# Performance work log

Hardware: AMD Instinct MI355X
Metric: run time of the kernel (lower is better)

The kernel has to match this reference:

```python
import jax, jax.numpy as jnp
import numpy as np

B, N, C_IN, C_OUT, BASIS = 8, 128, 64, 64, 15
AVG_NOBJ = 49.0
NEG_SLOPE = 0.01  # torch LeakyReLU default


def eops_2_to_2_sum(x, average_nobj=AVG_NOBJ):
    """x: [B, C, N, N] -> [B, C, 15, N, N].
    5 order-zero ops + 10 sum-aggregation ops (sums normalized by average_nobj,
    double sums by average_nobj**2, as in PELICAN's 'sum' aggregation)."""
    n = x.shape[-1]
    eye = jnp.eye(n, dtype=x.dtype)                       # [N, N]
    d = jnp.diagonal(x, axis1=-2, axis2=-1)               # [B, C, N]
    rowsum = x.sum(-1) / average_nobj                      # [B, C, N]
    colsum = x.sum(-2) / average_nobj                      # [B, C, N]
    trace = d.sum(-1) / average_nobj                       # [B, C]
    allsum = x.sum((-2, -1)) / (average_nobj ** 2)         # [B, C]
    bc = lambda v: jnp.broadcast_to(v, x.shape)
    ops = [
        # --- order zero (no aggregation) ---
        d[..., :, None] * eye,                 # diag(A) embedded on diagonal
        bc(d[..., :, None]),                   # A_ii broadcast along j
        bc(d[..., None, :]),                   # A_jj broadcast along i
        x,                                     # identity
        jnp.swapaxes(x, -1, -2),               # transpose
        # --- aggregation ops ---
        rowsum[..., :, None] * eye,            # row sums on diagonal
        colsum[..., :, None] * eye,            # col sums on diagonal
        trace[..., None, None] * eye,          # trace on diagonal
        allsum[..., None, None] * eye,         # total sum on diagonal
        bc(rowsum[..., :, None]),              # rowsum_i broadcast along j
        bc(rowsum[..., None, :]),              # rowsum_j broadcast along i
        bc(colsum[..., :, None]),              # colsum_i broadcast along j
        bc(colsum[..., None, :]),              # colsum_j broadcast along i
        bc(trace[..., None, None]),            # trace broadcast everywhere
        bc(allsum[..., None, None]),           # total sum broadcast everywhere
    ]
    return jnp.stack(ops, axis=2)              # [B, C, 15, N, N]


def setup_inputs() -> dict:
    key = jax.random.key(0)
    ks = jax.random.split(key, 5)
    inputs = jax.random.normal(ks[0], (B, N, N, C_IN), jnp.float32)
    mask = jnp.ones((B, N, N, 1), jnp.float32)
    nobj = jnp.full((B,), float(N), jnp.float32)
    s_b = float(np.sqrt(1.0 / BASIS))
    s_d = float(np.sqrt(1.0 / C_IN))
    coefs00 = jax.random.normal(ks[1], (C_IN, BASIS), jnp.float32) * s_b
    coefs01 = jax.random.normal(ks[2], (C_OUT, BASIS), jnp.float32) * s_b
    coefs10 = jax.random.normal(ks[3], (C_IN, C_OUT), jnp.float32) * s_d
    coefs11 = jax.random.normal(ks[4], (C_IN, C_OUT), jnp.float32) * s_d
    bias = jnp.zeros((C_OUT,), jnp.float32)
    diag_bias = jnp.zeros((C_OUT,), jnp.float32)
    return {"inputs": inputs, "mask": mask, "nobj": nobj,
            "coefs00": coefs00, "coefs01": coefs01,
            "coefs10": coefs10, "coefs11": coefs11,
            "bias": bias, "diag_bias": diag_bias}


def reference(inputs, mask, nobj, coefs00, coefs01, coefs10, coefs11, bias, diag_bias):
    # inputs: [B, N, N, C_in] -> channels-first for basis construction
    x = jnp.transpose(inputs, (0, 3, 1, 2))                     # [B, C, N, N]
    ops = eops_2_to_2_sum(x)                                    # [B, C, 15, N, N]
    # low-rank reconstructed coefficient tensor [C_in, C_out, 15]
    coefs = (coefs00[:, None, :] * coefs10[:, :, None]
             + coefs01[None, :, :] * coefs11[:, :, None])
    out = jnp.einsum('dsb,ndbij->nijs', coefs, ops)             # [B, N, N, C_out]
    eye = jnp.eye(inputs.shape[1], dtype=out.dtype)[None, :, :, None]
    out = out + bias[None, None, None, :] + eye * diag_bias[None, None, None, :]
    out = jax.nn.leaky_relu(out, NEG_SLOPE)
    return out * mask
```

## Files before the change

### kernel.cpp

```cpp
#include <hip/hip_runtime.h>

#define BB 8
#define NN 128
#define CC 64
static constexpr float INV_A = 1.0f / 49.0f;

#define OFF_C    0
#define OFF_CB   61440
#define OFF_RS   65536
#define OFF_CS   131072
#define OFF_DV   196608
#define OFF_U1   263168
#define OFF_U2   328704
#define OFF_DG   394240
#define OFF_XT   459776
#define OFF_TR   4654080
#define OFF_AS   4654592

typedef __attribute__((ext_vector_type(8))) short v8s;
typedef __attribute__((ext_vector_type(4))) float v4f;

static __device__ inline unsigned pack2bf(float a, float b) {
    union { float f; unsigned u; } ua, ub; ua.f = a; ub.f = b;
    return ((ua.u + 0x8000u) >> 16) | ((ub.u + 0x8000u) & 0xffff0000u);
}
static __device__ inline unsigned short f2bf(float a) {
    union { float f; unsigned u; } ua; ua.f = a;
    return (unsigned short)((ua.u + 0x8000u) >> 16);
}

__global__ void k_pre(const float* __restrict__ in,
                      const float* __restrict__ c00, const float* __restrict__ c01,
                      const float* __restrict__ c10, const float* __restrict__ c11,
                      float* __restrict__ ws) {
    if (blockIdx.x >= 512) {
        int idx = (blockIdx.x - 512) * 256 + threadIdx.x;
        if (idx < 15 * 4096) {
            int b = idx >> 12; int r = idx & 4095; int d = r >> 6; int s = r & 63;
            ws[OFF_C + idx] = c00[d * 15 + b] * c10[d * 64 + s] + c01[s * 15 + b] * c11[d * 64 + s];
        } else if (idx < 15 * 4096 + 8192) {
            int k = idx - 15 * 4096;
            int which = k >> 12;
            int r = k & 4095; int s = r >> 6; int d = r & 63;
            int b = 3 + which;
            float v = c00[d * 15 + b] * c10[d * 64 + s] + c01[s * 15 + b] * c11[d * 64 + s];
            unsigned short* cb = (unsigned short*)(ws + OFF_CB);
            cb[s * 128 + which * 64 + d] = f2bf(v);
        }
        return;
    }
    __shared__ float4 part[4][4][16];
    int mode = blockIdx.x >> 8;
    int bb = blockIdx.x & 255;
    int n = bb >> 5; int g0 = (bb & 31) * 4;
    int t = threadIdx.x;
    int q = t >> 6; int ii = (t >> 4) & 3; int d4 = t & 15;
    float4 acc = make_float4(0.f, 0.f, 0.f, 0.f);
    if (mode == 0) {
        int i = g0 + ii;
        float4 dvv = acc; bool hd = false;
        const float* base = in + ((size_t)(n * NN + i)) * NN * CC + d4 * 4;
        for (int j = q * 32; j < q * 32 + 32; ++j) {
            float4 v = *(const float4*)(base + (size_t)j * CC);
            acc.x += v.x; acc.y += v.y; acc.z += v.z; acc.w += v.w;
            if (j == i) { dvv = v; hd = true; }
        }
        if (hd) *(float4*)(ws + OFF_DV + ((size_t)(n * NN + i)) * CC + d4 * 4) = dvv;
    } else {
        int j = g0 + ii;
        unsigned short* xT = (unsigned short*)(ws + OFF_XT);
        for (int i = q * 32; i < q * 32 + 32; ++i) {
            float4 v = *(const float4*)(in + (((size_t)(n * NN + i)) * NN + j) * CC + d4 * 4);
            acc.x += v.x; acc.y += v.y; acc.z += v.z; acc.w += v.w;
            uint2 pk; pk.x = pack2bf(v.x, v.y); pk.y = pack2bf(v.z, v.w);
            *(uint2*)(xT + (((size_t)(n * NN + j)) * NN + i) * CC + d4 * 4) = pk;
        }
    }
    part[q][ii][d4] = acc;
    __syncthreads();
    if (t < 64) {
        int i2 = t >> 4; int dd = t & 15;
        float4 a = part[0][i2][dd], b = part[1][i2][dd], c = part[2][i2][dd], d = part[3][i2][dd];
        float4 s;
        s.x = (a.x + b.x + c.x + d.x) * INV_A;
        s.y = (a.y + b.y + c.y + d.y) * INV_A;
        s.z = (a.z + b.z + c.z + d.z) * INV_A;
        s.w = (a.w + b.w + c.w + d.w) * INV_A;
        *(float4*)(ws + (mode ? OFF_CS : OFF_RS) + ((size_t)(n * NN + g0 + i2)) * CC + dd * 4) = s;
    }
}

__global__ void k_tr(float* __restrict__ ws) {
    __shared__ float p[4][64][2];
    int n = blockIdx.x; int t = threadIdx.x;
    int s = t & 63; int iq = t >> 6;
    float tr = 0.f, as = 0.f;
    #pragma unroll 4
    for (int e = 0; e < 32; ++e) {
        int i = iq * 32 + e;
        tr += ws[OFF_DV + ((size_t)(n * NN + i)) * CC + s];
        as += ws[OFF_RS + ((size_t)(n * NN + i)) * CC + s];
    }
    p[iq][s][0] = tr; p[iq][s][1] = as;
    __syncthreads();
    if (t < 64) {
        ws[OFF_TR + n * 64 + t] = (p[0][t][0] + p[1][t][0] + p[2][t][0] + p[3][t][0]) * INV_A;
        ws[OFF_AS + n * 64 + t] = (p[0][t][1] + p[1][t][1] + p[2][t][1] + p[3][t][1]) * INV_A;
    }
}

__global__ __launch_bounds__(256, 4) void k_uv(const float* __restrict__ bias,
                                               const float* __restrict__ dbias,
                                               float* __restrict__ ws) {
    __shared__ float trL[64], asL[64];
    __shared__ float pU1[4][2][64], pU2[4][2][64], pDG[4][2][64];
    __shared__ float pS[4][64], pDGc[4][64];
    int n = blockIdx.x >> 6; int i0 = (blockIdx.x & 63) * 2;
    int t = threadIdx.x;
    int s = t & 63; int q = t >> 6;

    if (t < 64) trL[t] = ws[OFF_TR + n * 64 + t];
    else if (t < 128) asL[t - 64] = ws[OFF_AS + n * 64 + (t - 64)];
    __syncthreads();

    const float* C = ws + OFF_C;
    float aU1[2] = {0, 0}, aU2[2] = {0, 0}, aDG[2] = {0, 0};
    float aS = 0.f, aDGc = 0.f;
    #pragma unroll
    for (int c4 = 0; c4 < 4; ++c4) {
        int dc = q * 4 + c4;
        float tr4[4], as4[4], dv4[2][4], rs4[2][4], cs4[2][4];
        #pragma unroll
        for (int k = 0; k < 4; ++k) { tr4[k] = trL[dc * 4 + k]; as4[k] = asL[dc * 4 + k]; }
        #pragma unroll
        for (int ii = 0; ii < 2; ++ii) {
            size_t ro = ((size_t)(n * NN + i0 + ii)) * CC + dc * 4;
            float4 v = *(const float4*)(ws + OFF_DV + ro);
            dv4[ii][0] = v.x; dv4[ii][1] = v.y; dv4[ii][2] = v.z; dv4[ii][3] = v.w;
            float4 r = *(const float4*)(ws + OFF_RS + ro);
            rs4[ii][0] = r.x; rs4[ii][1] = r.y; rs4[ii][2] = r.z; rs4[ii][3] = r.w;
            float4 c = *(const float4*)(ws + OFF_CS + ro);
            cs4[ii][0] = c.x; cs4[ii][1] = c.y; cs4[ii][2] = c.z; cs4[ii][3] = c.w;
        }
        #pragma unroll
        for (int k = 0; k < 4; ++k) {
            int d = dc * 4 + k;
            const float* Cd = C + d * 64 + s;
            float c0 = Cd[0 * 4096], c1 = Cd[1 * 4096], c2 = Cd[2 * 4096];
            float c5 = Cd[5 * 4096], c6 = Cd[6 * 4096], c7 = Cd[7 * 4096];
            float c8 = Cd[8 * 4096], c9 = Cd[9 * 4096], c10v = Cd[10 * 4096];
            float c11v = Cd[11 * 4096], c12v = Cd[12 * 4096];
            float c13 = Cd[13 * 4096], c14 = Cd[14 * 4096];
            aS += c13 * tr4[k] + c14 * as4[k];
            aDGc += c7 * tr4[k] + c8 * as4[k];
            #pragma unroll
            for (int ii = 0; ii < 2; ++ii) {
                aU1[ii] += c1 * dv4[ii][k] + c9 * rs4[ii][k] + c11v * cs4[ii][k];
                aU2[ii] += c2 * dv4[ii][k] + c10v * rs4[ii][k] + c12v * cs4[ii][k];
                aDG[ii] += c0 * dv4[ii][k] + c5 * rs4[ii][k] + c6 * cs4[ii][k];
            }
        }
    }
    #pragma unroll
    for (int ii = 0; ii < 2; ++ii) {
        pU1[q][ii][s] = aU1[ii]; pU2[q][ii][s] = aU2[ii]; pDG[q][ii][s] = aDG[ii];
    }
    pS[q][s] = aS; pDGc[q][s] = aDGc;
    __syncthreads();

    if (t < 128) {
        int fi = t >> 6; int s2 = t & 63;
        float u1 = pU1[0][fi][s2] + pU1[1][fi][s2] + pU1[2][fi][s2] + pU1[3][fi][s2];
        float u2 = pU2[0][fi][s2] + pU2[1][fi][s2] + pU2[2][fi][s2] + pU2[3][fi][s2];
        float dg = pDG[0][fi][s2] + pDG[1][fi][s2] + pDG[2][fi][s2] + pDG[3][fi][s2];
        float aSt = pS[0][s2] + pS[1][s2] + pS[2][s2] + pS[3][s2];
        float aDGct = pDGc[0][s2] + pDGc[1][s2] + pDGc[2][s2] + pDGc[3][s2];
        size_t row = ((size_t)(n * NN + i0 + fi)) * CC + s2;
        ws[OFF_U1 + row] = u1 + aSt + bias[s2];
        ws[OFF_U2 + row] = u2;
        ws[OFF_DG + row] = dg + aDGct + dbias[s2];
    }
}

__global__ __launch_bounds__(256, 4) void k_main(
        const float* __restrict__ in, const float* __restrict__ mask,
        const float* __restrict__ ws, float* __restrict__ out) {
    __shared__ __align__(16) unsigned char smem[34816];
    unsigned short* Ab = (unsigned short*)smem;
    unsigned short* Bb = (unsigned short*)(smem + 17408);
    float* Obuf = (float*)smem;

    int blk = blockIdx.x;
    int n = blk >> 8; int rem = blk & 255; int i = rem >> 1; int j0 = (rem & 1) * 64;
    int t = threadIdx.x;
    int tp = t >> 4; int c = t & 15;

    const unsigned short* cb = (const unsigned short*)(ws + OFF_CB);
    #pragma unroll
    for (int e = 0; e < 4; ++e) {
        int s = e * 16 + tp;
        float4 v = *(const float4*)(cb + s * 128 + c * 8);
        *(float4*)((unsigned char*)(Bb + s * 136 + c * 8)) = v;
    }
    {
        const float* src = in + (((size_t)(n * NN + i)) * NN + j0) * CC;
        #pragma unroll
        for (int e = 0; e < 4; ++e) {
            int p = e * 16 + tp;
            float4 v = *(const float4*)(src + (size_t)p * CC + c * 4);
            uint2 pk; pk.x = pack2bf(v.x, v.y); pk.y = pack2bf(v.z, v.w);
            *(uint2*)(Ab + p * 136 + c * 4) = pk;
        }
    }
    {
        const unsigned short* xT = (const unsigned short*)(ws + OFF_XT)
                                 + (((size_t)(n * NN + i)) * NN + j0) * CC;
        #pragma unroll
        for (int r = 0; r < 2; ++r) {
            int idx = t + r * 256;
            int p = idx >> 3; int ch = idx & 7;
            float4 v = *(const float4*)(xT + (size_t)p * CC + ch * 8);
            *(float4*)((unsigned char*)(Ab + p * 136 + 64 + ch * 8)) = v;
        }
    }
    __syncthreads();

    int w = t >> 6; int l = t & 63;
    int r16 = l & 15; int quad = l >> 4;
    v4f acc[4];
    #pragma unroll
    for (int st = 0; st < 4; ++st) acc[st] = 0.f;
    int arow = w * 16 + r16;
    #pragma unroll
    for (int kk = 0; kk < 4; ++kk) {
        v8s af = *(const v8s*)(Ab + arow * 136 + kk * 32 + quad * 8);
        #pragma unroll
        for (int st = 0; st < 4; ++st) {
            v8s bfr = *(const v8s*)(Bb + (st * 16 + r16) * 136 + kk * 32 + quad * 8);
            acc[st] = __builtin_amdgcn_mfma_f32_16x16x32_bf16(af, bfr, acc[st], 0, 0, 0);
        }
    }
    #pragma unroll
    for (int st = 0; st < 4; ++st)
        #pragma unroll
        for (int reg = 0; reg < 4; ++reg)
            Obuf[(w * 16 + quad * 4 + reg) * 68 + st * 16 + r16] = acc[st][reg];
    __syncthreads();

    int srow = (n * NN + i) * CC;
    float4 u1 = *(const float4*)(ws + OFF_U1 + srow + c * 4);
    float4 dg = *(const float4*)(ws + OFF_DG + srow + c * 4);
    #pragma unroll
    for (int e = 0; e < 4; ++e) {
        int p = e * 16 + tp;
        int j = j0 + p;
        float4 v = *(const float4*)(Obuf + p * 68 + c * 4);
        float4 u2 = *(const float4*)(ws + OFF_U2 + (n * NN + j) * CC + c * 4);
        v.x += u1.x + u2.x; v.y += u1.y + u2.y; v.z += u1.z + u2.z; v.w += u1.w + u2.w;
        if (j == i) { v.x += dg.x; v.y += dg.y; v.z += dg.z; v.w += dg.w; }
        v.x = v.x > 0.f ? v.x : 0.01f * v.x;
        v.y = v.y > 0.f ? v.y : 0.01f * v.y;
        v.z = v.z > 0.f ? v.z : 0.01f * v.z;
        v.w = v.w > 0.f ? v.w : 0.01f * v.w;
        float m = mask[((size_t)(n * NN + i)) * NN + j];
        v.x *= m; v.y *= m; v.z *= m; v.w *= m;
        *(float4*)(out + (((size_t)(n * NN + i)) * NN + j) * CC + c * 4) = v;
    }
}

extern "C" void kernel_launch(void* const* d_in, const int* in_sizes, int n_in,
                              void* d_out, int out_size, void* d_ws, size_t ws_size,
                              hipStream_t stream) {
    const float* inputs = (const float*)d_in[0];
    const float* mask   = (const float*)d_in[1];
    const float* c00 = (const float*)d_in[3];
    const float* c01 = (const float*)d_in[4];
    const float* c10 = (const float*)d_in[5];
    const float* c11 = (const float*)d_in[6];
    const float* bias  = (const float*)d_in[7];
    const float* dbias = (const float*)d_in[8];
    float* out = (float*)d_out;
    float* ws = (float*)d_ws;

    k_pre <<<784, 256, 0, stream>>>(inputs, c00, c01, c10, c11, ws);
    k_tr  <<<8,   256, 0, stream>>>(ws);
    k_uv  <<<512, 256, 0, stream>>>(bias, dbias, ws);
    k_main<<<2048, 256, 0, stream>>>(inputs, mask, ws, out);
}
```

Measured before the change: 140.1 us.

## Drop transposed bf16 staging buffer and fold trace kernel into k_uv

k_pre no longer writes a transposed bf16 copy of the input. k_main now reads the transposed tile directly from the fp32 input with strided float4 loads and packs it to bf16 itself. The separate k_tr launch is removed: each k_uv block recomputes the per-batch trace and total sum from the diagonal and row-sum buffers. This removes a large workspace write and read plus one kernel launch, at the cost of less coalesced transposed loads in k_main and redundant reductions across the 64 k_uv blocks per batch.

```diff
diff --git a/kernel.cpp b/kernel.cpp
--- a/kernel.cpp
+++ b/kernel.cpp
@@ -13,9 +13,6 @@
 #define OFF_U1   263168
 #define OFF_U2   328704
 #define OFF_DG   394240
-#define OFF_XT   459776
-#define OFF_TR   4654080
-#define OFF_AS   4654592
 
 typedef __attribute__((ext_vector_type(8))) short v8s;
 typedef __attribute__((ext_vector_type(4))) float v4f;
@@ -68,12 +65,9 @@
         if (hd) *(float4*)(ws + OFF_DV + ((size_t)(n * NN + i)) * CC + d4 * 4) = dvv;
     } else {
         int j = g0 + ii;
-        unsigned short* xT = (unsigned short*)(ws + OFF_XT);
         for (int i = q * 32; i < q * 32 + 32; ++i) {
             float4 v = *(const float4*)(in + (((size_t)(n * NN + i)) * NN + j) * CC + d4 * 4);
             acc.x += v.x; acc.y += v.y; acc.z += v.z; acc.w += v.w;
-            uint2 pk; pk.x = pack2bf(v.x, v.y); pk.y = pack2bf(v.z, v.w);
-            *(uint2*)(xT + (((size_t)(n * NN + j)) * NN + i) * CC + d4 * 4) = pk;
         }
     }
     part[q][ii][d4] = acc;
@@ -90,25 +84,6 @@
     }
 }
 
-__global__ void k_tr(float* __restrict__ ws) {
-    __shared__ float p[4][64][2];
-    int n = blockIdx.x; int t = threadIdx.x;
-    int s = t & 63; int iq = t >> 6;
-    float tr = 0.f, as = 0.f;
-    #pragma unroll 4
-    for (int e = 0; e < 32; ++e) {
-        int i = iq * 32 + e;
-        tr += ws[OFF_DV + ((size_t)(n * NN + i)) * CC + s];
-        as += ws[OFF_RS + ((size_t)(n * NN + i)) * CC + s];
-    }
-    p[iq][s][0] = tr; p[iq][s][1] = as;
-    __syncthreads();
-    if (t < 64) {
-        ws[OFF_TR + n * 64 + t] = (p[0][t][0] + p[1][t][0] + p[2][t][0] + p[3][t][0]) * INV_A;
-        ws[OFF_AS + n * 64 + t] = (p[0][t][1] + p[1][t][1] + p[2][t][1] + p[3][t][1]) * INV_A;
-    }
-}
-
 __global__ __launch_bounds__(256, 4) void k_uv(const float* __restrict__ bias,
                                                const float* __restrict__ dbias,
                                                float* __restrict__ ws) {
@@ -119,9 +94,22 @@
     int t = threadIdx.x;
     int s = t & 63; int q = t >> 6;
 
-    if (t < 64) trL[t] = ws[OFF_TR + n * 64 + t];
-    else if (t < 128) asL[t - 64] = ws[OFF_AS + n * 64 + (t - 64)];
-    __syncthreads();
+    {
+        float tr = 0.f, as = 0.f;
+        #pragma unroll 4
+        for (int e = 0; e < 32; ++e) {
+            int i = q * 32 + e;
+            tr += ws[OFF_DV + ((size_t)(n * NN + i)) * CC + s];
+            as += ws[OFF_RS + ((size_t)(n * NN + i)) * CC + s];
+        }
+        pS[q][s] = tr; pDGc[q][s] = as;
+        __syncthreads();
+        if (t < 64) {
+            trL[t] = (pS[0][t] + pS[1][t] + pS[2][t] + pS[3][t]) * INV_A;
+            asL[t] = (pDGc[0][t] + pDGc[1][t] + pDGc[2][t] + pDGc[3][t]) * INV_A;
+        }
+        __syncthreads();
+    }
 
     const float* C = ws + OFF_C;
     float aU1[2] = {0, 0}, aU2[2] = {0, 0}, aDG[2] = {0, 0};
@@ -213,14 +201,14 @@
         }
     }
     {
-        const unsigned short* xT = (const unsigned short*)(ws + OFF_XT)
-                                 + (((size_t)(n * NN + i)) * NN + j0) * CC;
-        #pragma unroll
-        for (int r = 0; r < 2; ++r) {
+        const float* srcT = in + ((size_t)(n * NN + j0) * NN + i) * CC;
+        #pragma unroll
+        for (int r = 0; r < 4; ++r) {
             int idx = t + r * 256;
-            int p = idx >> 3; int ch = idx & 7;
-            float4 v = *(const float4*)(xT + (size_t)p * CC + ch * 8);
-            *(float4*)((unsigned char*)(Ab + p * 136 + 64 + ch * 8)) = v;
+            int p = idx >> 4; int cq = idx & 15;
+            float4 v = *(const float4*)(srcT + (size_t)p * NN * CC + cq * 4);
+            uint2 pk; pk.x = pack2bf(v.x, v.y); pk.y = pack2bf(v.z, v.w);
+            *(uint2*)(Ab + p * 136 + 64 + cq * 4) = pk;
         }
     }
     __syncthreads();
@@ -283,7 +271,6 @@
     float* ws = (float*)d_ws;
 
     k_pre <<<784, 256, 0, stream>>>(inputs, c00, c01, c10, c11, ws);
-    k_tr  <<<8,   256, 0, stream>>>(ws);
     k_uv  <<<512, 256, 0, stream>>>(bias, dbias, ws);
     k_main<<<2048, 256, 0, stream>>>(inputs, mask, ws, out);
 }
```

Result: no change. 139.4 us (-0.5%).
